# Kernel tuning notes

Hardware: AMD Instinct MI355X
Metric: run time of the kernel (lower is better)

Reference implementation:

```python
import jax, jax.numpy as jnp
import numpy as np

INPUT_SIZE = 32
HIDDEN_SIZE = 128
N_HEAD = 8
NER_NUMS = 8
D = INPUT_SIZE * NER_NUMS  # 256, attention feature dim per head


def setup_inputs() -> dict:
    key = jax.random.key(0)
    ks = jax.random.split(key, 10)
    B, S = 8, 2048
    x = jax.random.normal(ks[0], (B, S, D), dtype=jnp.float32)
    bi_lstm_o = jax.random.normal(ks[1], (B, S, 2 * HIDDEN_SIZE), dtype=jnp.float32)
    # per-head linear params, stacked on leading head axis (nn.init.normal_ -> std 1)
    Qw = jax.random.normal(ks[2], (N_HEAD, 2 * HIDDEN_SIZE, D), dtype=jnp.float32)
    Qb = jax.random.normal(ks[3], (N_HEAD, D), dtype=jnp.float32)
    Kw = jax.random.normal(ks[4], (N_HEAD, D, D), dtype=jnp.float32)
    Kb = jax.random.normal(ks[5], (N_HEAD, D), dtype=jnp.float32)
    Vw = jax.random.normal(ks[6], (N_HEAD, D, D), dtype=jnp.float32)
    Vb = jax.random.normal(ks[7], (N_HEAD, D), dtype=jnp.float32)
    Cw = jax.random.normal(ks[8], (N_HEAD * D, NER_NUMS), dtype=jnp.float32)
    Cb = jax.random.normal(ks[9], (NER_NUMS,), dtype=jnp.float32)
    return {"x": x, "bi_lstm_o": bi_lstm_o, "Qw": Qw, "Qb": Qb, "Kw": Kw,
            "Kb": Kb, "Vw": Vw, "Vb": Vb, "Cw": Cw, "Cb": Cb}


def reference(x, bi_lstm_o, Qw, Qb, Kw, Kb, Vw, Vb, Cw, Cb):
    # q from bi_lstm_o, k/v from x; all heads batched on axis h
    q = jnp.einsum('bsf,hfd->hbsd', bi_lstm_o, Qw) + Qb[:, None, None, :]
    k = jnp.einsum('bsf,hfd->hbsd', x, Kw) + Kb[:, None, None, :]
    v = jnp.einsum('bsf,hfd->hbsd', x, Vw) + Vb[:, None, None, :]
    scale = 1.0 / jnp.sqrt(jnp.float32(D))
    scores = jnp.einsum('hbsd,hbtd->hbst', q, k) * scale  # [H,B,S,S]
    attn = jax.nn.softmax(scores, axis=-1)
    o = jnp.einsum('hbst,hbtd->hbsd', attn, v)  # [H,B,S,D]
    B, S = x.shape[0], x.shape[1]
    concat = jnp.transpose(o, (1, 2, 0, 3)).reshape(B, S, N_HEAD * D)  # head order matches torch.cat
    return concat @ Cw + Cb
```

## Files before the change

### kernel.cpp

```cpp
#include <hip/hip_runtime.h>

#define H_ 8
#define B_ 8
#define S_ 2048
#define D_ 256

#define KSTRIDE 264
#define VSTRIDE 40

typedef __attribute__((ext_vector_type(8))) _Float16 half8;
typedef __attribute__((ext_vector_type(4))) _Float16 half4v;
typedef __attribute__((ext_vector_type(2))) _Float16 half2v;
typedef __attribute__((ext_vector_type(4))) float f32x4;

__device__ inline void split8(const float* __restrict__ p, half8& hv, half8& lv) {
  float4 a = *(const float4*)p, b = *(const float4*)(p + 4);
  hv[0] = (_Float16)a.x; hv[1] = (_Float16)a.y; hv[2] = (_Float16)a.z; hv[3] = (_Float16)a.w;
  hv[4] = (_Float16)b.x; hv[5] = (_Float16)b.y; hv[6] = (_Float16)b.z; hv[7] = (_Float16)b.w;
  lv[0] = (_Float16)(a.x - (float)hv[0]); lv[1] = (_Float16)(a.y - (float)hv[1]);
  lv[2] = (_Float16)(a.z - (float)hv[2]); lv[3] = (_Float16)(a.w - (float)hv[3]);
  lv[4] = (_Float16)(b.x - (float)hv[4]); lv[5] = (_Float16)(b.y - (float)hv[5]);
  lv[6] = (_Float16)(b.z - (float)hv[6]); lv[7] = (_Float16)(b.w - (float)hv[7]);
}

__global__ void split_w_kernel(const float* __restrict__ W,
                               _Float16* __restrict__ thi, _Float16* __restrict__ tlo) {
  __shared__ float t[64][65];
  const int h = blockIdx.z, f0 = blockIdx.x * 64, d0 = blockIdx.y * 64;
  const int col = threadIdx.x & 63, rg = threadIdx.x >> 6;
#pragma unroll
  for (int it = 0; it < 16; ++it) {
    int f = rg * 16 + it;
    t[f][col] = W[((size_t)h * 256 + f0 + f) * 256 + d0 + col];
  }
  __syncthreads();
#pragma unroll
  for (int it = 0; it < 16; ++it) {
    int d = rg * 16 + it;
    float v = t[col][d];
    _Float16 hv = (_Float16)v;
    size_t idx = ((size_t)h * 256 + d0 + d) * 256 + f0 + col;
    thi[idx] = hv;
    tlo[idx] = (_Float16)(v - (float)hv);
  }
}

__global__ void out_init_kernel(float* __restrict__ out, const float* __restrict__ Cb) {
  int i = blockIdx.x * blockDim.x + threadIdx.x;
  if (i < B_ * S_ * 8) out[i] = Cb[i & 7];
}

template <int VMODE>
__global__ __launch_bounds__(256, 2) void proj_kernel(
    const float* __restrict__ A,
    const _Float16* __restrict__ Whi, const _Float16* __restrict__ Wlo,
    const float* __restrict__ bias, float oscale, int h0,
    _Float16* __restrict__ Ohi, _Float16* __restrict__ Olo) {
  constexpr bool TMULT = (VMODE != 1);
  __shared__ _Float16 a_hi[128 * VSTRIDE] __attribute__((aligned(16)));
  __shared__ _Float16 b_hi[128 * VSTRIDE] __attribute__((aligned(16)));
  __shared__ _Float16 a_lo[TMULT ? 128 * VSTRIDE : 8] __attribute__((aligned(16)));
  __shared__ _Float16 b_lo[TMULT ? 128 * VSTRIDE : 8] __attribute__((aligned(16)));
  const int tid = threadIdx.x;
  const int w = tid >> 6, lane = tid & 63;
  const int quad = lane >> 4, l15 = lane & 15;
  const int hb = blockIdx.z, h = h0 + (hb >> 3), b = hb & 7;
  const int s0 = blockIdx.x * 128, d0 = blockIdx.y * 128;
  const int wr = w >> 1, wc = w & 1;
  const f32x4 fz = {0.f, 0.f, 0.f, 0.f};
  f32x4 acc[4][4];
#pragma unroll
  for (int i = 0; i < 4; ++i)
#pragma unroll
    for (int j = 0; j < 4; ++j) acc[i][j] = fz;
  const size_t arow0 = (size_t)b * S_ + s0;
  const size_t wrow0 = (size_t)h * 256 + d0;
  for (int kk = 0; kk < 8; ++kk) {
    const int f0 = kk * 32;
    __syncthreads();
#pragma unroll
    for (int i = 0; i < 2; ++i) {
      int cc = i * 256 + tid;
      int r = cc >> 2, ch = (cc & 3) * 8;
      half8 hv, lv;
      split8(A + (arow0 + r) * 256 + f0 + ch, hv, lv);
      *(half8*)&a_hi[r * VSTRIDE + ch] = hv;
      size_t woff = (wrow0 + r) * 256 + f0 + ch;
      *(half8*)&b_hi[r * VSTRIDE + ch] = *(const half8*)(Whi + woff);
      if (TMULT) {
        *(half8*)&a_lo[r * VSTRIDE + ch] = lv;
        *(half8*)&b_lo[r * VSTRIDE + ch] = *(const half8*)(Wlo + woff);
      }
    }
    __syncthreads();
    half8 afh[4], afl[4], bfh[4], bfl[4];
#pragma unroll
    for (int t = 0; t < 4; ++t) {
      int ar = wr * 64 + t * 16 + l15;
      afh[t] = *(const half8*)&a_hi[ar * VSTRIDE + quad * 8];
      int br = wc * 64 + t * 16 + l15;
      bfh[t] = *(const half8*)&b_hi[br * VSTRIDE + quad * 8];
      if (TMULT) {
        afl[t] = *(const half8*)&a_lo[ar * VSTRIDE + quad * 8];
        bfl[t] = *(const half8*)&b_lo[br * VSTRIDE + quad * 8];
      }
    }
#pragma unroll
    for (int rf = 0; rf < 4; ++rf)
#pragma unroll
      for (int cf = 0; cf < 4; ++cf) {
        acc[rf][cf] = __builtin_amdgcn_mfma_f32_16x16x32_f16(afh[rf], bfh[cf], acc[rf][cf], 0, 0, 0);
        if (TMULT) {
          acc[rf][cf] = __builtin_amdgcn_mfma_f32_16x16x32_f16(afh[rf], bfl[cf], acc[rf][cf], 0, 0, 0);
          acc[rf][cf] = __builtin_amdgcn_mfma_f32_16x16x32_f16(afl[rf], bfh[cf], acc[rf][cf], 0, 0, 0);
        }
      }
  }
#pragma unroll
  for (int rf = 0; rf < 4; ++rf) {
#pragma unroll
    for (int cf = 0; cf < 4; ++cf) {
      const int d = d0 + wc * 64 + cf * 16 + l15;
      const float bv = bias[h * 256 + d];
      if (VMODE != 1) {
#pragma unroll
        for (int r = 0; r < 4; ++r) {
          const int s = s0 + wr * 64 + rf * 16 + quad * 4 + r;
          float val = (acc[rf][cf][r] + bv) * oscale;
          _Float16 hvv = (_Float16)val;
          size_t idx = ((size_t)hb * S_ + s) * 256 + d;
          Ohi[idx] = hvv;
          if (VMODE == 0) Olo[idx] = (_Float16)(val - (float)hvv);
        }
      } else {
        half4v pack;
#pragma unroll
        for (int r = 0; r < 4; ++r) pack[r] = (_Float16)((acc[rf][cf][r] + bv) * oscale);
        size_t idx = ((size_t)hb * 256 + d) * S_ + s0 + wr * 64 + rf * 16 + quad * 4;
        *(half4v*)(Ohi + idx) = pack;
      }
    }
  }
}

__global__ __launch_bounds__(256, 2) void flash_kernel(
    const _Float16* __restrict__ qhi, const _Float16* __restrict__ qlo,
    const _Float16* __restrict__ khi,
    const _Float16* __restrict__ vt, const float* __restrict__ Cw,
    float* __restrict__ out, int h0) {
  __shared__ _Float16 khi_s[32 * KSTRIDE] __attribute__((aligned(16)));
  __shared__ _Float16 vt_s[256 * VSTRIDE] __attribute__((aligned(16)));
  __shared__ _Float16 p_s[4][16 * VSTRIDE] __attribute__((aligned(16)));
  const int tid = threadIdx.x, w = tid >> 6, lane = tid & 63;
  const int quad = lane >> 4, l15 = lane & 15;
  const int hb = blockIdx.y, h = h0 + (hb >> 3), b = hb & 7;
  const int qbase = blockIdx.x * 64;
  half8 qfh[8], qfl[8];
  {
    size_t qrow = (size_t)hb * S_ + qbase + w * 16 + l15;
    const _Float16* qh = qhi + qrow * 256 + quad * 8;
    const _Float16* ql = qlo + qrow * 256 + quad * 8;
#pragma unroll
    for (int ks = 0; ks < 8; ++ks) {
      qfh[ks] = *(const half8*)(qh + ks * 32);
      qfl[ks] = *(const half8*)(ql + ks * 32);
    }
  }
  const f32x4 fz = {0.f, 0.f, 0.f, 0.f};
  f32x4 o_acc[16];
#pragma unroll
  for (int df = 0; df < 16; ++df) o_acc[df] = fz;
  float m_r = -3.0e38f, l_r = 0.f;

  for (int kt = 0; kt < 64; ++kt) {
    __syncthreads();
    {
      size_t kbase = ((size_t)hb * S_ + kt * 32) * 256;
#pragma unroll
      for (int i = 0; i < 4; ++i) {
        int cc = i * 256 + tid;
        int kr = cc >> 5, kch = (cc & 31) * 8;
        *(half8*)&khi_s[kr * KSTRIDE + kch] = *(const half8*)(khi + kbase + kr * 256 + kch);
        int vd = cc >> 2, vch = (cc & 3) * 8;
        size_t voff = ((size_t)hb * 256 + vd) * S_ + kt * 32 + vch;
        *(half8*)&vt_s[vd * VSTRIDE + vch] = *(const half8*)(vt + voff);
      }
    }
    __syncthreads();
    f32x4 sc0 = fz, sc1 = fz;
#pragma unroll
    for (int ks = 0; ks < 8; ++ks) {
      half8 bh0 = *(const half8*)&khi_s[(0 * 16 + l15) * KSTRIDE + ks * 32 + quad * 8];
      sc0 = __builtin_amdgcn_mfma_f32_16x16x32_f16(bh0, qfh[ks], sc0, 0, 0, 0);
      sc0 = __builtin_amdgcn_mfma_f32_16x16x32_f16(bh0, qfl[ks], sc0, 0, 0, 0);
      half8 bh1 = *(const half8*)&khi_s[(1 * 16 + l15) * KSTRIDE + ks * 32 + quad * 8];
      sc1 = __builtin_amdgcn_mfma_f32_16x16x32_f16(bh1, qfh[ks], sc1, 0, 0, 0);
      sc1 = __builtin_amdgcn_mfma_f32_16x16x32_f16(bh1, qfl[ks], sc1, 0, 0, 0);
    }
    float v = fmaxf(fmaxf(fmaxf(sc0[0], sc0[1]), fmaxf(sc0[2], sc0[3])),
                    fmaxf(fmaxf(sc1[0], sc1[1]), fmaxf(sc1[2], sc1[3])));
    v = fmaxf(v, __shfl_xor(v, 16));
    v = fmaxf(v, __shfl_xor(v, 32));
    const float mn = fmaxf(m_r, v);
    const float al = __expf(m_r - mn);
    m_r = mn;
    float p0[4], p1[4], s = 0.f;
#pragma unroll
    for (int r = 0; r < 4; ++r) {
      p0[r] = __expf(sc0[r] - mn);
      p1[r] = __expf(sc1[r] - mn);
      s += p0[r] + p1[r];
    }
    s += __shfl_xor(s, 16);
    s += __shfl_xor(s, 32);
    l_r = l_r * al + s;
    {
      _Float16* pb = &p_s[w][l15 * VSTRIDE + quad * 4];
      half2v w0 = {(_Float16)p0[0], (_Float16)p0[1]};
      half2v w1 = {(_Float16)p0[2], (_Float16)p0[3]};
      half2v w2 = {(_Float16)p1[0], (_Float16)p1[1]};
      half2v w3 = {(_Float16)p1[2], (_Float16)p1[3]};
      *(half2v*)(pb) = w0;
      *(half2v*)(pb + 2) = w1;
      *(half2v*)(pb + 16) = w2;
      *(half2v*)(pb + 18) = w3;
    }
    float al_r[4];
#pragma unroll
    for (int r = 0; r < 4; ++r) al_r[r] = __shfl(al, quad * 4 + r);
#pragma unroll
    for (int df = 0; df < 16; ++df)
#pragma unroll
      for (int r = 0; r < 4; ++r) o_acc[df][r] *= al_r[r];
    __syncthreads();
    half8 pf = *(const half8*)&p_s[w][l15 * VSTRIDE + quad * 8];
#pragma unroll
    for (int df = 0; df < 16; ++df) {
      half8 vf = *(const half8*)&vt_s[(df * 16 + l15) * VSTRIDE + quad * 8];
      o_acc[df] = __builtin_amdgcn_mfma_f32_16x16x32_f16(pf, vf, o_acc[df], 0, 0, 0);
    }
  }
  float rcl[4];
#pragma unroll
  for (int r = 0; r < 4; ++r) rcl[r] = 1.0f / __shfl(l_r, quad * 4 + r);
  float part[32];
#pragma unroll
  for (int i = 0; i < 32; ++i) part[i] = 0.f;
#pragma unroll
  for (int df = 0; df < 16; ++df) {
    const float4* cwv = (const float4*)(Cw + ((size_t)h * 256 + df * 16 + l15) * 8);
    float4 c0 = cwv[0], c1 = cwv[1];
#pragma unroll
    for (int r = 0; r < 4; ++r) {
      float ov = o_acc[df][r] * rcl[r];
      part[r * 8 + 0] += ov * c0.x;
      part[r * 8 + 1] += ov * c0.y;
      part[r * 8 + 2] += ov * c0.z;
      part[r * 8 + 3] += ov * c0.w;
      part[r * 8 + 4] += ov * c1.x;
      part[r * 8 + 5] += ov * c1.y;
      part[r * 8 + 6] += ov * c1.z;
      part[r * 8 + 7] += ov * c1.w;
    }
  }
#pragma unroll
  for (int i = 0; i < 32; ++i) {
    float v = part[i];
    v += __shfl_xor(v, 1);
    v += __shfl_xor(v, 2);
    v += __shfl_xor(v, 4);
    v += __shfl_xor(v, 8);
    part[i] = v;
  }
  if (l15 == 0) {
#pragma unroll
    for (int r = 0; r < 4; ++r) {
      int s = qbase + w * 16 + quad * 4 + r;
#pragma unroll
      for (int j = 0; j < 8; ++j)
        atomicAdd(&out[((size_t)b * S_ + s) * 8 + j], part[r * 8 + j]);
    }
  }
}

extern "C" void kernel_launch(void* const* d_in, const int* in_sizes, int n_in,
                              void* d_out, int out_size, void* d_ws, size_t ws_size,
                              hipStream_t stream) {
  const float* x  = (const float*)d_in[0];
  const float* bo = (const float*)d_in[1];
  const float* Qw = (const float*)d_in[2];
  const float* Qb = (const float*)d_in[3];
  const float* Kw = (const float*)d_in[4];
  const float* Kb = (const float*)d_in[5];
  const float* Vw = (const float*)d_in[6];
  const float* Vb = (const float*)d_in[7];
  const float* Cw = (const float*)d_in[8];
  const float* Cb = (const float*)d_in[9];
  float* out = (float*)d_out;

  const size_t NW  = (size_t)H_ * 256 * 256;
  const size_t NHB = (size_t)B_ * S_ * 256;
  const size_t ALN = 256;
  auto pad = [](size_t b) { return (b + 255) & ~(size_t)255; };

  int HC = 8;
  while (HC > 1) {
    size_t need = 6 * pad(NW * 2) + 4 * pad((size_t)HC * NHB * 2) + ALN;
    if (need <= ws_size) break;
    HC >>= 1;
  }

  char* base = (char*)d_ws;
  size_t off = 0;
  auto carve = [&](size_t nelem) -> _Float16* {
    _Float16* p = (_Float16*)(base + off);
    off += pad(nelem * 2);
    return p;
  };
  _Float16* qwt_hi = carve(NW); _Float16* qwt_lo = carve(NW);
  _Float16* kwt_hi = carve(NW); _Float16* kwt_lo = carve(NW);
  _Float16* vwt_hi = carve(NW); _Float16* vwt_lo = carve(NW);
  const size_t NC = (size_t)HC * NHB;
  _Float16* q_hi = carve(NC); _Float16* q_lo = carve(NC);
  _Float16* k_hi = carve(NC);
  _Float16* v_t  = carve(NC);

  dim3 wg(4, 4, 8);
  split_w_kernel<<<wg, 256, 0, stream>>>(Qw, qwt_hi, qwt_lo);
  split_w_kernel<<<wg, 256, 0, stream>>>(Kw, kwt_hi, kwt_lo);
  split_w_kernel<<<wg, 256, 0, stream>>>(Vw, vwt_hi, vwt_lo);
  out_init_kernel<<<(B_ * S_ * 8) / 256, 256, 0, stream>>>(out, Cb);

  for (int h0 = 0; h0 < H_; h0 += HC) {
    dim3 pg(16, 2, HC * 8);
    proj_kernel<0><<<pg, 256, 0, stream>>>(bo, qwt_hi, qwt_lo, Qb, 0.0625f, h0, q_hi, q_lo);
    proj_kernel<2><<<pg, 256, 0, stream>>>(x, kwt_hi, kwt_lo, Kb, 1.0f, h0, k_hi, nullptr);
    proj_kernel<1><<<pg, 256, 0, stream>>>(x, vwt_hi, vwt_lo, Vb, 1.0f, h0, v_t, nullptr);
    dim3 fg(32, HC * 8);
    flash_kernel<<<fg, 256, 0, stream>>>(q_hi, q_lo, k_hi, v_t, Cw, out, h0);
  }
}
```

Before: 918.8 us.

## Rewrite projection GEMM to hold weight slices in registers, drop LDS staging

The projection kernel no longer stages A and W tiles through shared memory with barriers. Each block now keeps a 32-column weight slice (hi and lo parts) resident in registers and streams activation rows straight from global memory into the MFMAs. The grid is remapped to batch × (d-chunk, s-chunk) × head. This removes LDS traffic and syncs, but each block reloads A once per 32-column d-chunk (8x redundant A reads) and raises register pressure.

```diff
diff --git a/kernel.cpp b/kernel.cpp
--- a/kernel.cpp
+++ b/kernel.cpp
@@ -57,88 +57,85 @@
     const float* __restrict__ bias, float oscale, int h0,
     _Float16* __restrict__ Ohi, _Float16* __restrict__ Olo) {
   constexpr bool TMULT = (VMODE != 1);
-  __shared__ _Float16 a_hi[128 * VSTRIDE] __attribute__((aligned(16)));
-  __shared__ _Float16 b_hi[128 * VSTRIDE] __attribute__((aligned(16)));
-  __shared__ _Float16 a_lo[TMULT ? 128 * VSTRIDE : 8] __attribute__((aligned(16)));
-  __shared__ _Float16 b_lo[TMULT ? 128 * VSTRIDE : 8] __attribute__((aligned(16)));
   const int tid = threadIdx.x;
   const int w = tid >> 6, lane = tid & 63;
   const int quad = lane >> 4, l15 = lane & 15;
-  const int hb = blockIdx.z, h = h0 + (hb >> 3), b = hb & 7;
-  const int s0 = blockIdx.x * 128, d0 = blockIdx.y * 128;
-  const int wr = w >> 1, wc = w & 1;
+  const int b = blockIdx.x;
+  const int dchunk = blockIdx.y & 7, schunk = blockIdx.y >> 3;
+  const int h = h0 + blockIdx.z;
+  const int hb = blockIdx.z * 8 + b;
+  const int d0 = dchunk * 32;
+  half8 wh[2][8], wl[2][8];
+  {
+    const size_t wbase = ((size_t)h * 256 + d0 + l15) * 256 + quad * 8;
+#pragma unroll
+    for (int c = 0; c < 2; ++c)
+#pragma unroll
+      for (int ks = 0; ks < 8; ++ks) {
+        size_t woff = wbase + (size_t)c * 16 * 256 + ks * 32;
+        wh[c][ks] = *(const half8*)(Whi + woff);
+        if constexpr (TMULT) wl[c][ks] = *(const half8*)(Wlo + woff);
+      }
+  }
+  const float bv0 = bias[h * 256 + d0 + l15];
+  const float bv1 = bias[h * 256 + d0 + 16 + l15];
   const f32x4 fz = {0.f, 0.f, 0.f, 0.f};
-  f32x4 acc[4][4];
-#pragma unroll
-  for (int i = 0; i < 4; ++i)
-#pragma unroll
-    for (int j = 0; j < 4; ++j) acc[i][j] = fz;
-  const size_t arow0 = (size_t)b * S_ + s0;
-  const size_t wrow0 = (size_t)h * 256 + d0;
-  for (int kk = 0; kk < 8; ++kk) {
-    const int f0 = kk * 32;
-    __syncthreads();
-#pragma unroll
-    for (int i = 0; i < 2; ++i) {
-      int cc = i * 256 + tid;
-      int r = cc >> 2, ch = (cc & 3) * 8;
-      half8 hv, lv;
-      split8(A + (arow0 + r) * 256 + f0 + ch, hv, lv);
-      *(half8*)&a_hi[r * VSTRIDE + ch] = hv;
-      size_t woff = (wrow0 + r) * 256 + f0 + ch;
-      *(half8*)&b_hi[r * VSTRIDE + ch] = *(const half8*)(Whi + woff);
-      if (TMULT) {
-        *(half8*)&a_lo[r * VSTRIDE + ch] = lv;
-        *(half8*)&b_lo[r * VSTRIDE + ch] = *(const half8*)(Wlo + woff);
-      }
-    }
-    __syncthreads();
-    half8 afh[4], afl[4], bfh[4], bfl[4];
-#pragma unroll
-    for (int t = 0; t < 4; ++t) {
-      int ar = wr * 64 + t * 16 + l15;
-      afh[t] = *(const half8*)&a_hi[ar * VSTRIDE + quad * 8];
-      int br = wc * 64 + t * 16 + l15;
-      bfh[t] = *(const half8*)&b_hi[br * VSTRIDE + quad * 8];
-      if (TMULT) {
-        afl[t] = *(const half8*)&a_lo[ar * VSTRIDE + quad * 8];
-        bfl[t] = *(const half8*)&b_lo[br * VSTRIDE + quad * 8];
-      }
-    }
-#pragma unroll
-    for (int rf = 0; rf < 4; ++rf)
-#pragma unroll
-      for (int cf = 0; cf < 4; ++cf) {
-        acc[rf][cf] = __builtin_amdgcn_mfma_f32_16x16x32_f16(afh[rf], bfh[cf], acc[rf][cf], 0, 0, 0);
-        if (TMULT) {
-          acc[rf][cf] = __builtin_amdgcn_mfma_f32_16x16x32_f16(afh[rf], bfl[cf], acc[rf][cf], 0, 0, 0);
-          acc[rf][cf] = __builtin_amdgcn_mfma_f32_16x16x32_f16(afl[rf], bfh[cf], acc[rf][cf], 0, 0, 0);
+  const float* pa = A + ((size_t)b * S_ + schunk * 512 + w * 16 + l15) * 256 + quad * 8;
+  for (int t = 0; t < 8; ++t) {
+    const float* pat = pa + (size_t)t * 64 * 256;
+    f32x4 acc0 = fz, acc1 = fz;
+#pragma unroll
+    for (int ks = 0; ks < 8; ++ks) {
+      half8 ah, al;
+      if constexpr (TMULT) {
+        split8(pat + ks * 32, ah, al);
+      } else {
+        float4 a0 = *(const float4*)(pat + ks * 32);
+        float4 a1 = *(const float4*)(pat + ks * 32 + 4);
+        ah[0] = (_Float16)a0.x; ah[1] = (_Float16)a0.y; ah[2] = (_Float16)a0.z; ah[3] = (_Float16)a0.w;
+        ah[4] = (_Float16)a1.x; ah[5] = (_Float16)a1.y; ah[6] = (_Float16)a1.z; ah[7] = (_Float16)a1.w;
+      }
+      acc0 = __builtin_amdgcn_mfma_f32_16x16x32_f16(ah, wh[0][ks], acc0, 0, 0, 0);
+      if constexpr (TMULT) {
+        acc0 = __builtin_amdgcn_mfma_f32_16x16x32_f16(ah, wl[0][ks], acc0, 0, 0, 0);
+        acc0 = __builtin_amdgcn_mfma_f32_16x16x32_f16(al, wh[0][ks], acc0, 0, 0, 0);
+      }
+      acc1 = __builtin_amdgcn_mfma_f32_16x16x32_f16(ah, wh[1][ks], acc1, 0, 0, 0);
+      if constexpr (TMULT) {
+        acc1 = __builtin_amdgcn_mfma_f32_16x16x32_f16(ah, wl[1][ks], acc1, 0, 0, 0);
+        acc1 = __builtin_amdgcn_mfma_f32_16x16x32_f16(al, wh[1][ks], acc1, 0, 0, 0);
+      }
+    }
+    const int srow = schunk * 512 + t * 64 + w * 16 + quad * 4;
+    if constexpr (VMODE != 1) {
+#pragma unroll
+      for (int r = 0; r < 4; ++r) {
+        {
+          float val = (acc0[r] + bv0) * oscale;
+          _Float16 hv = (_Float16)val;
+          size_t idx = ((size_t)hb * S_ + srow + r) * 256 + d0 + l15;
+          Ohi[idx] = hv;
+          if constexpr (VMODE == 0) Olo[idx] = (_Float16)(val - (float)hv);
         }
-      }
-  }
-#pragma unroll
-  for (int rf = 0; rf < 4; ++rf) {
-#pragma unroll
-    for (int cf = 0; cf < 4; ++cf) {
-      const int d = d0 + wc * 64 + cf * 16 + l15;
-      const float bv = bias[h * 256 + d];
-      if (VMODE != 1) {
-#pragma unroll
-        for (int r = 0; r < 4; ++r) {
-          const int s = s0 + wr * 64 + rf * 16 + quad * 4 + r;
-          float val = (acc[rf][cf][r] + bv) * oscale;
-          _Float16 hvv = (_Float16)val;
-          size_t idx = ((size_t)hb * S_ + s) * 256 + d;
-          Ohi[idx] = hvv;
-          if (VMODE == 0) Olo[idx] = (_Float16)(val - (float)hvv);
+        {
+          float val = (acc1[r] + bv1) * oscale;
+          _Float16 hv = (_Float16)val;
+          size_t idx = ((size_t)hb * S_ + srow + r) * 256 + d0 + 16 + l15;
+          Ohi[idx] = hv;
+          if constexpr (VMODE == 0) Olo[idx] = (_Float16)(val - (float)hv);
         }
-      } else {
-        half4v pack;
-#pragma unroll
-        for (int r = 0; r < 4; ++r) pack[r] = (_Float16)((acc[rf][cf][r] + bv) * oscale);
-        size_t idx = ((size_t)hb * 256 + d) * S_ + s0 + wr * 64 + rf * 16 + quad * 4;
-        *(half4v*)(Ohi + idx) = pack;
-      }
+      }
+    } else {
+      half4v p0, p1;
+#pragma unroll
+      for (int r = 0; r < 4; ++r) {
+        p0[r] = (_Float16)((acc0[r] + bv0) * oscale);
+        p1[r] = (_Float16)((acc1[r] + bv1) * oscale);
+      }
+      size_t i0 = ((size_t)hb * 256 + d0 + l15) * S_ + srow;
+      size_t i1 = ((size_t)hb * 256 + d0 + 16 + l15) * S_ + srow;
+      *(half4v*)(Ohi + i0) = p0;
+      *(half4v*)(Ohi + i1) = p1;
     }
   }
 }
@@ -332,7 +329,7 @@
   out_init_kernel<<<(B_ * S_ * 8) / 256, 256, 0, stream>>>(out, Cb);
 
   for (int h0 = 0; h0 < H_; h0 += HC) {
-    dim3 pg(16, 2, HC * 8);
+    dim3 pg(8, 32, HC);
     proj_kernel<0><<<pg, 256, 0, stream>>>(bo, qwt_hi, qwt_lo, Qb, 0.0625f, h0, q_hi, q_lo);
     proj_kernel<2><<<pg, 256, 0, stream>>>(x, kwt_hi, kwt_lo, Kb, 1.0f, h0, k_hi, nullptr);
     proj_kernel<1><<<pg, 256, 0, stream>>>(x, vwt_hi, vwt_lo, Vb, 1.0f, h0, v_t, nullptr);
```

After: 1.175 ms. +27.9%, slower.

## Process two 16-row query groups per wave in flash kernel to reuse K/V tiles

Applied to the files above, without the earlier changes.

Each wave now handles 32 query rows (two 16-row groups) instead of 16, so each block covers 128 queries and the grid halves. K and V fragments read from shared memory are reused across both groups, halving K/V global and LDS traffic per query. In exchange, register use roughly doubles for accumulators and Q fragments, so launch bounds drop to one block per SM-equivalent, lowering occupancy and parallelism with fewer blocks.

```diff
diff --git a/kernel.cpp b/kernel.cpp
--- a/kernel.cpp
+++ b/kernel.cpp
@@ -143,34 +143,39 @@
   }
 }
 
-__global__ __launch_bounds__(256, 2) void flash_kernel(
+__global__ __launch_bounds__(256, 1) void flash_kernel(
     const _Float16* __restrict__ qhi, const _Float16* __restrict__ qlo,
     const _Float16* __restrict__ khi,
     const _Float16* __restrict__ vt, const float* __restrict__ Cw,
     float* __restrict__ out, int h0) {
   __shared__ _Float16 khi_s[32 * KSTRIDE] __attribute__((aligned(16)));
   __shared__ _Float16 vt_s[256 * VSTRIDE] __attribute__((aligned(16)));
-  __shared__ _Float16 p_s[4][16 * VSTRIDE] __attribute__((aligned(16)));
+  __shared__ _Float16 p_s[4][2][16 * VSTRIDE] __attribute__((aligned(16)));
   const int tid = threadIdx.x, w = tid >> 6, lane = tid & 63;
   const int quad = lane >> 4, l15 = lane & 15;
   const int hb = blockIdx.y, h = h0 + (hb >> 3), b = hb & 7;
-  const int qbase = blockIdx.x * 64;
-  half8 qfh[8], qfl[8];
-  {
-    size_t qrow = (size_t)hb * S_ + qbase + w * 16 + l15;
+  const int qbase = blockIdx.x * 128 + w * 32;
+  half8 qfh[2][8], qfl[2][8];
+#pragma unroll
+  for (int g = 0; g < 2; ++g) {
+    size_t qrow = (size_t)hb * S_ + qbase + g * 16 + l15;
     const _Float16* qh = qhi + qrow * 256 + quad * 8;
     const _Float16* ql = qlo + qrow * 256 + quad * 8;
 #pragma unroll
     for (int ks = 0; ks < 8; ++ks) {
-      qfh[ks] = *(const half8*)(qh + ks * 32);
-      qfl[ks] = *(const half8*)(ql + ks * 32);
+      qfh[g][ks] = *(const half8*)(qh + ks * 32);
+      qfl[g][ks] = *(const half8*)(ql + ks * 32);
     }
   }
   const f32x4 fz = {0.f, 0.f, 0.f, 0.f};
-  f32x4 o_acc[16];
-#pragma unroll
-  for (int df = 0; df < 16; ++df) o_acc[df] = fz;
-  float m_r = -3.0e38f, l_r = 0.f;
+  f32x4 o_acc[2][16];
+#pragma unroll
+  for (int g = 0; g < 2; ++g)
+#pragma unroll
+    for (int df = 0; df < 16; ++df) o_acc[g][df] = fz;
+  float m_r[2], l_r[2];
+#pragma unroll
+  for (int g = 0; g < 2; ++g) { m_r[g] = -3.0e38f; l_r[g] = 0.f; }
 
   for (int kt = 0; kt < 64; ++kt) {
     __syncthreads();
@@ -187,35 +192,43 @@
       }
     }
     __syncthreads();
-    f32x4 sc0 = fz, sc1 = fz;
+    f32x4 sc0[2], sc1[2];
+#pragma unroll
+    for (int g = 0; g < 2; ++g) { sc0[g] = fz; sc1[g] = fz; }
 #pragma unroll
     for (int ks = 0; ks < 8; ++ks) {
       half8 bh0 = *(const half8*)&khi_s[(0 * 16 + l15) * KSTRIDE + ks * 32 + quad * 8];
-      sc0 = __builtin_amdgcn_mfma_f32_16x16x32_f16(bh0, qfh[ks], sc0, 0, 0, 0);
-      sc0 = __builtin_amdgcn_mfma_f32_16x16x32_f16(bh0, qfl[ks], sc0, 0, 0, 0);
       half8 bh1 = *(const half8*)&khi_s[(1 * 16 + l15) * KSTRIDE + ks * 32 + quad * 8];
-      sc1 = __builtin_amdgcn_mfma_f32_16x16x32_f16(bh1, qfh[ks], sc1, 0, 0, 0);
-      sc1 = __builtin_amdgcn_mfma_f32_16x16x32_f16(bh1, qfl[ks], sc1, 0, 0, 0);
-    }
-    float v = fmaxf(fmaxf(fmaxf(sc0[0], sc0[1]), fmaxf(sc0[2], sc0[3])),
-                    fmaxf(fmaxf(sc1[0], sc1[1]), fmaxf(sc1[2], sc1[3])));
-    v = fmaxf(v, __shfl_xor(v, 16));
-    v = fmaxf(v, __shfl_xor(v, 32));
-    const float mn = fmaxf(m_r, v);
-    const float al = __expf(m_r - mn);
-    m_r = mn;
-    float p0[4], p1[4], s = 0.f;
-#pragma unroll
-    for (int r = 0; r < 4; ++r) {
-      p0[r] = __expf(sc0[r] - mn);
-      p1[r] = __expf(sc1[r] - mn);
-      s += p0[r] + p1[r];
-    }
-    s += __shfl_xor(s, 16);
-    s += __shfl_xor(s, 32);
-    l_r = l_r * al + s;
-    {
-      _Float16* pb = &p_s[w][l15 * VSTRIDE + quad * 4];
+#pragma unroll
+      for (int g = 0; g < 2; ++g) {
+        sc0[g] = __builtin_amdgcn_mfma_f32_16x16x32_f16(bh0, qfh[g][ks], sc0[g], 0, 0, 0);
+        sc0[g] = __builtin_amdgcn_mfma_f32_16x16x32_f16(bh0, qfl[g][ks], sc0[g], 0, 0, 0);
+        sc1[g] = __builtin_amdgcn_mfma_f32_16x16x32_f16(bh1, qfh[g][ks], sc1[g], 0, 0, 0);
+        sc1[g] = __builtin_amdgcn_mfma_f32_16x16x32_f16(bh1, qfl[g][ks], sc1[g], 0, 0, 0);
+      }
+    }
+    float al_g[2];
+#pragma unroll
+    for (int g = 0; g < 2; ++g) {
+      float v = fmaxf(fmaxf(fmaxf(sc0[g][0], sc0[g][1]), fmaxf(sc0[g][2], sc0[g][3])),
+                      fmaxf(fmaxf(sc1[g][0], sc1[g][1]), fmaxf(sc1[g][2], sc1[g][3])));
+      v = fmaxf(v, __shfl_xor(v, 16));
+      v = fmaxf(v, __shfl_xor(v, 32));
+      const float mn = fmaxf(m_r[g], v);
+      const float al = __expf(m_r[g] - mn);
+      m_r[g] = mn;
+      float p0[4], p1[4], s = 0.f;
+#pragma unroll
+      for (int r = 0; r < 4; ++r) {
+        p0[r] = __expf(sc0[g][r] - mn);
+        p1[r] = __expf(sc1[g][r] - mn);
+        s += p0[r] + p1[r];
+      }
+      s += __shfl_xor(s, 16);
+      s += __shfl_xor(s, 32);
+      l_r[g] = l_r[g] * al + s;
+      al_g[g] = al;
+      _Float16* pb = &p_s[w][g][l15 * VSTRIDE + quad * 4];
       half2v w0 = {(_Float16)p0[0], (_Float16)p0[1]};
       half2v w1 = {(_Float16)p0[2], (_Float16)p0[3]};
       half2v w2 = {(_Float16)p1[0], (_Float16)p1[1]};
@@ -225,60 +238,68 @@
       *(half2v*)(pb + 16) = w2;
       *(half2v*)(pb + 18) = w3;
     }
-    float al_r[4];
-#pragma unroll
-    for (int r = 0; r < 4; ++r) al_r[r] = __shfl(al, quad * 4 + r);
-#pragma unroll
-    for (int df = 0; df < 16; ++df)
-#pragma unroll
-      for (int r = 0; r < 4; ++r) o_acc[df][r] *= al_r[r];
-    __syncthreads();
-    half8 pf = *(const half8*)&p_s[w][l15 * VSTRIDE + quad * 8];
+#pragma unroll
+    for (int g = 0; g < 2; ++g) {
+      float al_r[4];
+#pragma unroll
+      for (int r = 0; r < 4; ++r) al_r[r] = __shfl(al_g[g], quad * 4 + r);
+#pragma unroll
+      for (int df = 0; df < 16; ++df)
+#pragma unroll
+        for (int r = 0; r < 4; ++r) o_acc[g][df][r] *= al_r[r];
+    }
+    __syncthreads();
+    half8 pf0 = *(const half8*)&p_s[w][0][l15 * VSTRIDE + quad * 8];
+    half8 pf1 = *(const half8*)&p_s[w][1][l15 * VSTRIDE + quad * 8];
 #pragma unroll
     for (int df = 0; df < 16; ++df) {
       half8 vf = *(const half8*)&vt_s[(df * 16 + l15) * VSTRIDE + quad * 8];
-      o_acc[df] = __builtin_amdgcn_mfma_f32_16x16x32_f16(pf, vf, o_acc[df], 0, 0, 0);
-    }
-  }
-  float rcl[4];
-#pragma unroll
-  for (int r = 0; r < 4; ++r) rcl[r] = 1.0f / __shfl(l_r, quad * 4 + r);
-  float part[32];
-#pragma unroll
-  for (int i = 0; i < 32; ++i) part[i] = 0.f;
-#pragma unroll
-  for (int df = 0; df < 16; ++df) {
-    const float4* cwv = (const float4*)(Cw + ((size_t)h * 256 + df * 16 + l15) * 8);
-    float4 c0 = cwv[0], c1 = cwv[1];
-#pragma unroll
-    for (int r = 0; r < 4; ++r) {
-      float ov = o_acc[df][r] * rcl[r];
-      part[r * 8 + 0] += ov * c0.x;
-      part[r * 8 + 1] += ov * c0.y;
-      part[r * 8 + 2] += ov * c0.z;
-      part[r * 8 + 3] += ov * c0.w;
-      part[r * 8 + 4] += ov * c1.x;
-      part[r * 8 + 5] += ov * c1.y;
-      part[r * 8 + 6] += ov * c1.z;
-      part[r * 8 + 7] += ov * c1.w;
-    }
-  }
-#pragma unroll
-  for (int i = 0; i < 32; ++i) {
-    float v = part[i];
-    v += __shfl_xor(v, 1);
-    v += __shfl_xor(v, 2);
-    v += __shfl_xor(v, 4);
-    v += __shfl_xor(v, 8);
-    part[i] = v;
-  }
-  if (l15 == 0) {
-#pragma unroll
-    for (int r = 0; r < 4; ++r) {
-      int s = qbase + w * 16 + quad * 4 + r;
-#pragma unroll
-      for (int j = 0; j < 8; ++j)
-        atomicAdd(&out[((size_t)b * S_ + s) * 8 + j], part[r * 8 + j]);
+      o_acc[0][df] = __builtin_amdgcn_mfma_f32_16x16x32_f16(pf0, vf, o_acc[0][df], 0, 0, 0);
+      o_acc[1][df] = __builtin_amdgcn_mfma_f32_16x16x32_f16(pf1, vf, o_acc[1][df], 0, 0, 0);
+    }
+  }
+#pragma unroll
+  for (int g = 0; g < 2; ++g) {
+    float rcl[4];
+#pragma unroll
+    for (int r = 0; r < 4; ++r) rcl[r] = 1.0f / __shfl(l_r[g], quad * 4 + r);
+    float part[32];
+#pragma unroll
+    for (int i = 0; i < 32; ++i) part[i] = 0.f;
+#pragma unroll
+    for (int df = 0; df < 16; ++df) {
+      const float4* cwv = (const float4*)(Cw + ((size_t)h * 256 + df * 16 + l15) * 8);
+      float4 c0 = cwv[0], c1 = cwv[1];
+#pragma unroll
+      for (int r = 0; r < 4; ++r) {
+        float ov = o_acc[g][df][r] * rcl[r];
+        part[r * 8 + 0] += ov * c0.x;
+        part[r * 8 + 1] += ov * c0.y;
+        part[r * 8 + 2] += ov * c0.z;
+        part[r * 8 + 3] += ov * c0.w;
+        part[r * 8 + 4] += ov * c1.x;
+        part[r * 8 + 5] += ov * c1.y;
+        part[r * 8 + 6] += ov * c1.z;
+        part[r * 8 + 7] += ov * c1.w;
+      }
+    }
+#pragma unroll
+    for (int i = 0; i < 32; ++i) {
+      float v = part[i];
+      v += __shfl_xor(v, 1);
+      v += __shfl_xor(v, 2);
+      v += __shfl_xor(v, 4);
+      v += __shfl_xor(v, 8);
+      part[i] = v;
+    }
+    if (l15 == 0) {
+#pragma unroll
+      for (int r = 0; r < 4; ++r) {
+        int s = qbase + g * 16 + quad * 4 + r;
+#pragma unroll
+        for (int j = 0; j < 8; ++j)
+          atomicAdd(&out[((size_t)b * S_ + s) * 8 + j], part[r * 8 + j]);
+      }
     }
   }
 }
@@ -336,7 +357,7 @@
     proj_kernel<0><<<pg, 256, 0, stream>>>(bo, qwt_hi, qwt_lo, Qb, 0.0625f, h0, q_hi, q_lo);
     proj_kernel<2><<<pg, 256, 0, stream>>>(x, kwt_hi, kwt_lo, Kb, 1.0f, h0, k_hi, nullptr);
     proj_kernel<1><<<pg, 256, 0, stream>>>(x, vwt_hi, vwt_lo, Vb, 1.0f, h0, v_t, nullptr);
-    dim3 fg(32, HC * 8);
+    dim3 fg(16, HC * 8);
     flash_kernel<<<fg, 256, 0, stream>>>(q_hi, q_lo, k_hi, v_t, Cw, out, h0);
   }
 }
```

Result: slower. 1.056 ms (+15.0%).

## Fuse Q projection into flash attention kernel prologue

Applied to the files above, without the earlier changes.

Removes the separate Q projection kernel and its hi/lo fp16 Q buffers, and instead computes each block's 64 query rows inside the flash kernel with split-fp16 MFMA before the attention loop. This drops the global write and read of Q and one kernel launch, and halves the per-head-chunk workspace so more heads fit per pass. In exchange it adds an extra 20KB shared buffer, which may reduce occupancy. Register pressure also rises from the extra accumulator array, and the Q rows are rebuilt through shared memory with several extra barriers.

```diff
diff --git a/kernel.cpp b/kernel.cpp
--- a/kernel.cpp
+++ b/kernel.cpp
@@ -7,6 +7,7 @@
 
 #define KSTRIDE 264
 #define VSTRIDE 40
+#define QTSTRIDE 136
 
 typedef __attribute__((ext_vector_type(8))) _Float16 half8;
 typedef __attribute__((ext_vector_type(4))) _Float16 half4v;
@@ -144,29 +145,87 @@
 }
 
 __global__ __launch_bounds__(256, 2) void flash_kernel(
-    const _Float16* __restrict__ qhi, const _Float16* __restrict__ qlo,
+    const float* __restrict__ bo,
+    const _Float16* __restrict__ qwhi, const _Float16* __restrict__ qwlo,
+    const float* __restrict__ qbias,
     const _Float16* __restrict__ khi,
     const _Float16* __restrict__ vt, const float* __restrict__ Cw,
     float* __restrict__ out, int h0) {
   __shared__ _Float16 khi_s[32 * KSTRIDE] __attribute__((aligned(16)));
   __shared__ _Float16 vt_s[256 * VSTRIDE] __attribute__((aligned(16)));
   __shared__ _Float16 p_s[4][16 * VSTRIDE] __attribute__((aligned(16)));
+  __shared__ _Float16 wbuf[256 * VSTRIDE] __attribute__((aligned(16)));
   const int tid = threadIdx.x, w = tid >> 6, lane = tid & 63;
   const int quad = lane >> 4, l15 = lane & 15;
   const int hb = blockIdx.y, h = h0 + (hb >> 3), b = hb & 7;
   const int qbase = blockIdx.x * 64;
+  _Float16* psf = &p_s[0][0];
+
+  const f32x4 fz = {0.f, 0.f, 0.f, 0.f};
+  f32x4 qacc[16];
+#pragma unroll
+  for (int df = 0; df < 16; ++df) qacc[df] = fz;
+  for (int kk = 0; kk < 8; ++kk) {
+    __syncthreads();
+#pragma unroll
+    for (int i = 0; i < 4; ++i) {
+      int c = i * 256 + tid;
+      int dr = c >> 2, ch = (c & 3) * 8;
+      size_t woff = ((size_t)h * 256 + dr) * 256 + kk * 32 + ch;
+      *(half8*)&vt_s[dr * VSTRIDE + ch] = *(const half8*)(qwhi + woff);
+      *(half8*)&wbuf[dr * VSTRIDE + ch] = *(const half8*)(qwlo + woff);
+    }
+    {
+      int rrow = tid >> 2, ch = (tid & 3) * 8;
+      half8 hv, lv;
+      split8(bo + ((size_t)b * S_ + qbase + rrow) * 256 + kk * 32 + ch, hv, lv);
+      *(half8*)&khi_s[rrow * VSTRIDE + ch] = hv;
+      *(half8*)&psf[rrow * VSTRIDE + ch] = lv;
+    }
+    __syncthreads();
+    half8 bh = *(const half8*)&khi_s[(w * 16 + l15) * VSTRIDE + quad * 8];
+    half8 bl = *(const half8*)&psf[(w * 16 + l15) * VSTRIDE + quad * 8];
+#pragma unroll
+    for (int df = 0; df < 16; ++df) {
+      half8 awh = *(const half8*)&vt_s[(df * 16 + l15) * VSTRIDE + quad * 8];
+      half8 awl = *(const half8*)&wbuf[(df * 16 + l15) * VSTRIDE + quad * 8];
+      qacc[df] = __builtin_amdgcn_mfma_f32_16x16x32_f16(awh, bh, qacc[df], 0, 0, 0);
+      qacc[df] = __builtin_amdgcn_mfma_f32_16x16x32_f16(awl, bh, qacc[df], 0, 0, 0);
+      qacc[df] = __builtin_amdgcn_mfma_f32_16x16x32_f16(awh, bl, qacc[df], 0, 0, 0);
+    }
+  }
   half8 qfh[8], qfl[8];
-  {
-    size_t qrow = (size_t)hb * S_ + qbase + w * 16 + l15;
-    const _Float16* qh = qhi + qrow * 256 + quad * 8;
-    const _Float16* ql = qlo + qrow * 256 + quad * 8;
-#pragma unroll
-    for (int ks = 0; ks < 8; ++ks) {
-      qfh[ks] = *(const half8*)(qh + ks * 32);
-      qfl[ks] = *(const half8*)(ql + ks * 32);
-    }
-  }
-  const f32x4 fz = {0.f, 0.f, 0.f, 0.f};
+#pragma unroll
+  for (int ph = 0; ph < 4; ++ph) {
+    const bool lo = ph >= 2;
+    const int dh = (ph & 1) * 8;
+    __syncthreads();
+#pragma unroll
+    for (int dfi = 0; dfi < 8; ++dfi) {
+      int df = dh + dfi;
+#pragma unroll
+      for (int rp = 0; rp < 2; ++rp) {
+        half2v hw;
+#pragma unroll
+        for (int rr = 0; rr < 2; ++rr) {
+          int r = rp * 2 + rr;
+          float bv = qbias[h * 256 + df * 16 + quad * 4 + r];
+          float val = (qacc[df][r] + bv) * 0.0625f;
+          _Float16 hv = (_Float16)val;
+          hw[rr] = lo ? (_Float16)(val - (float)hv) : hv;
+        }
+        *(half2v*)&vt_s[(w * 16 + l15) * QTSTRIDE + dfi * 16 + quad * 4 + rp * 2] = hw;
+      }
+    }
+    __syncthreads();
+#pragma unroll
+    for (int k2 = 0; k2 < 4; ++k2) {
+      half8 v = *(const half8*)&vt_s[(w * 16 + l15) * QTSTRIDE + k2 * 32 + quad * 8];
+      if (lo) qfl[(ph & 1) * 4 + k2] = v;
+      else    qfh[(ph & 1) * 4 + k2] = v;
+    }
+  }
+
   f32x4 o_acc[16];
 #pragma unroll
   for (int df = 0; df < 16; ++df) o_acc[df] = fz;
@@ -305,7 +364,7 @@
 
   int HC = 8;
   while (HC > 1) {
-    size_t need = 6 * pad(NW * 2) + 4 * pad((size_t)HC * NHB * 2) + ALN;
+    size_t need = 6 * pad(NW * 2) + 2 * pad((size_t)HC * NHB * 2) + ALN;
     if (need <= ws_size) break;
     HC >>= 1;
   }
@@ -321,7 +380,6 @@
   _Float16* kwt_hi = carve(NW); _Float16* kwt_lo = carve(NW);
   _Float16* vwt_hi = carve(NW); _Float16* vwt_lo = carve(NW);
   const size_t NC = (size_t)HC * NHB;
-  _Float16* q_hi = carve(NC); _Float16* q_lo = carve(NC);
   _Float16* k_hi = carve(NC);
   _Float16* v_t  = carve(NC);
 
@@ -333,10 +391,9 @@
 
   for (int h0 = 0; h0 < H_; h0 += HC) {
     dim3 pg(16, 2, HC * 8);
-    proj_kernel<0><<<pg, 256, 0, stream>>>(bo, qwt_hi, qwt_lo, Qb, 0.0625f, h0, q_hi, q_lo);
     proj_kernel<2><<<pg, 256, 0, stream>>>(x, kwt_hi, kwt_lo, Kb, 1.0f, h0, k_hi, nullptr);
     proj_kernel<1><<<pg, 256, 0, stream>>>(x, vwt_hi, vwt_lo, Vb, 1.0f, h0, v_t, nullptr);
     dim3 fg(32, HC * 8);
-    flash_kernel<<<fg, 256, 0, stream>>>(q_hi, q_lo, k_hi, v_t, Cw, out, h0);
-  }
-}
+    flash_kernel<<<fg, 256, 0, stream>>>(bo, qwt_hi, qwt_lo, Qb, k_hi, v_t, Cw, out, h0);
+  }
+}
```

Measured after the change: 837.0 us. -8.9%, faster.
